# Kernel optimization log

Hardware: AMD Instinct MI355X
Metric: run time of the kernel (lower is better)

## Reference

```python
import jax, jax.numpy as jnp
import numpy as np

# module hyperparameters (from init_kwargs)
DELTA_T = 300
K = 16
FS = 30
HIGH_PASS = 40  # bpm
LOW_PASS = 250  # bpm

# static frequency band selection: rfft length F = DELTA_T//2 + 1
_F = DELTA_T // 2 + 1
_freqs = np.linspace(0.0, FS / 2.0, _F)
_sel = np.nonzero((_freqs >= HIGH_PASS / 60.0) & (_freqs <= LOW_PASS / 60.0))[0]
SEL_LO, SEL_HI = int(_sel[0]), int(_sel[-1]) + 1  # contiguous band -> static slice


def setup_inputs() -> dict:
    key = jax.random.key(0)
    k1, k2 = jax.random.split(key)
    B, C, T = 128, 32, 9000
    x = jax.random.normal(k1, (B, C, T), dtype=jnp.float32)
    offsets = jax.random.randint(k2, (B, C, K), 0, T - DELTA_T + 1, dtype=jnp.int32)
    return {"x": x, "offsets": offsets}


def reference(x, offsets):
    # x: [B, C, T], offsets: [B, C, K] in [0, T - DELTA_T]
    # Gather K random windows of length DELTA_T per (b, c).
    idx = offsets[..., None] + jnp.arange(DELTA_T, dtype=offsets.dtype)  # [B,C,K,DT]
    w = jnp.take_along_axis(x[:, :, None, :], idx, axis=-1)             # [B,C,K,DT]
    # mean-subtract along time
    w = w - jnp.mean(w, axis=-1, keepdims=True)
    # rfft with norm='forward' (divide by N), power spectrum
    spec = jnp.fft.rfft(w, axis=-1, norm="forward")                     # [B,C,K,F]
    p = spec.real ** 2 + spec.imag ** 2
    # static band selection (freqs in [HIGH_PASS/60, LOW_PASS/60] Hz)
    p = p[..., SEL_LO:SEL_HI]                                           # [B,C,K,35]
    # normalize to unit sum -> normalized PSD
    return p / jnp.sum(p, axis=-1, keepdims=True)
```

## Files before the change

kernel.cpp:

```cpp
#include <hip/hip_runtime.h>
#include <hip/hip_bf16.h>

using frag_ab = __attribute__((ext_vector_type(8))) short;
using f32x4   = __attribute__((ext_vector_type(4))) float;
typedef float f32x4u __attribute__((ext_vector_type(4), aligned(4)));


struct CS { double c[300]; double s[300]; };

constexpr CS make_cs() {
    CS t{};
    const double PI = 3.14159265358979323846;
    for (int m = 0; m < 300; ++m) {
        int q = m / 75, r = m % 75;
        double th = PI * (double)r / 150.0;
        double x2 = th * th;
        double term = 1.0, cv = 0.0;
        for (int k2 = 0; k2 < 12; ++k2) { cv += term; term *= -x2 / ((2*k2+1)*(2*k2+2)); }
        double sv = 0.0; term = th;
        for (int k2 = 0; k2 < 12; ++k2) { sv += term; term *= -x2 / ((2*k2+2)*(2*k2+3)); }
        double cc = 0.0, ss = 0.0;
        if      (q == 0) { cc =  cv; ss =  sv; }
        else if (q == 1) { cc = -sv; ss =  cv; }
        else if (q == 2) { cc = -cv; ss = -sv; }
        else             { cc =  sv; ss = -cv; }
        t.c[m] = cc; t.s[m] = ss;
    }
    return t;
}
constexpr CS TAB = make_cs();

constexpr unsigned short d2bf(double v) {
    unsigned s = 0; double a = v;
    if (a < 0) { s = 1; a = -a; }
    if (a < 1e-8) return 0;
    int e = 0;
    while (a >= 2.0) { a *= 0.5; ++e; }
    while (a <  1.0) { a *= 2.0; --e; }
    double m = (a - 1.0) * 128.0;
    int mi = (int)(m + 0.5);
    int ef = 127 + e;
    if (mi == 128) { mi = 0; ++ef; }
    return (unsigned short)((s << 15) | ((unsigned)ef << 7) | (unsigned)mi);
}

struct alignas(16) Chunk { unsigned short v[2560]; };

constexpr Chunk make_chunk(int kc) {
    Chunk ch{};
    for (int i = 0; i < 2560; ++i) {
        int e = i & 7, l = (i >> 3) & 63, n = i >> 9;
        int k   = kc * 32 + ((l >> 4) << 3) + e;
        int col = n * 16 + (l & 15);
        double v = 0.0;
        if (k < 300 && col < 70) {
            int j = (col < 35) ? col : col - 35;
            int m = ((7 + j) * k) % 300;
            v = (col < 35) ? TAB.c[m] : TAB.s[m];
        }
        ch.v[i] = d2bf(v);
    }
    return ch;
}

__device__ constexpr Chunk BP0 = make_chunk(0);
__device__ constexpr Chunk BP1 = make_chunk(1);
__device__ constexpr Chunk BP2 = make_chunk(2);
__device__ constexpr Chunk BP3 = make_chunk(3);
__device__ constexpr Chunk BP4 = make_chunk(4);
__device__ constexpr Chunk BP5 = make_chunk(5);
__device__ constexpr Chunk BP6 = make_chunk(6);
__device__ constexpr Chunk BP7 = make_chunk(7);
__device__ constexpr Chunk BP8 = make_chunk(8);
__device__ constexpr Chunk BP9 = make_chunk(9);

__device__ __forceinline__ const unsigned short* bp_ptr(int kc) {
    switch (kc) {
        case 0: return BP0.v; case 1: return BP1.v; case 2: return BP2.v;
        case 3: return BP3.v; case 4: return BP4.v; case 5: return BP5.v;
        case 6: return BP6.v; case 7: return BP7.v; case 8: return BP8.v;
        default: return BP9.v;
    }
}

__device__ __forceinline__ unsigned short f2bf(float f) {
    unsigned u = __float_as_uint(f);
    u += 0x7fffu + ((u >> 16) & 1u);
    return (unsigned short)(u >> 16);
}

__global__ __launch_bounds__(256) void st_spec_main(
    const float* __restrict__ x, const int* __restrict__ offs,
    float* __restrict__ out)
{
    const int tid  = threadIdx.x;
    const int wave = tid >> 6;
    const int lane = tid & 63;
    const int bc   = blockIdx.x * 4 + wave;
    const int c16  = lane & 15;
    const int kq   = lane >> 4;

    const float* xrow = x + (size_t)bc * 9000;
    const int off = offs[bc * 16 + c16];

    frag_ab a[10];
    #pragma unroll
    for (int kc = 0; kc < 9; ++kc) {
        const float* p = xrow + off + kc * 32 + kq * 8;
        f32x4u v0 = *(const f32x4u*)p;
        f32x4u v1 = *(const f32x4u*)(p + 4);
        frag_ab av;
        #pragma unroll
        for (int e = 0; e < 4; ++e) av[e] = (short)f2bf(v0[e]);
        #pragma unroll
        for (int e = 0; e < 4; ++e) av[4 + e] = (short)f2bf(v1[e]);
        a[kc] = av;
    }
    {
        int tb = 288 + kq * 8;
        frag_ab av;
        #pragma unroll
        for (int e = 0; e < 8; ++e) {
            int t = tb + e;
            av[e] = (short)f2bf((t < 300) ? xrow[off + t] : 0.0f);
        }
        a[9] = av;
    }

    f32x4 acc[5];
    #pragma unroll
    for (int n = 0; n < 5; ++n) acc[n] = (f32x4){0.f, 0.f, 0.f, 0.f};

    #pragma unroll
    for (int kc = 0; kc < 10; ++kc) {
        const unsigned short* bp = bp_ptr(kc);
        #pragma unroll
        for (int n = 0; n < 5; ++n) {
            frag_ab b = *(const frag_ab*)&bp[(n * 64 + lane) * 8];
            acc[n] = __builtin_amdgcn_mfma_f32_16x16x32_bf16(a[kc], b, acc[n], 0, 0, 0);
        }
    }

    const int src = (lane & 48) | ((c16 + 3) & 15);
    #pragma unroll
    for (int r = 0; r < 4; ++r) {
        float re0 = acc[0][r], re1 = acc[1][r], re2 = acc[2][r];
        float sh2 = __shfl(acc[2][r], src);
        float sh3 = __shfl(acc[3][r], src);
        float sh4 = __shfl(acc[4][r], src);
        float im0 = (c16 < 13) ? sh2 : sh3;
        float im1 = (c16 < 13) ? sh3 : sh4;
        float p0 = re0 * re0 + im0 * im0;
        float p1 = re1 * re1 + im1 * im1;
        float p2 = (c16 < 3) ? (re2 * re2 + sh4 * sh4) : 0.0f;
        float ps = p0 + p1 + p2;
        ps += __shfl_xor(ps, 1);
        ps += __shfl_xor(ps, 2);
        ps += __shfl_xor(ps, 4);
        ps += __shfl_xor(ps, 8);
        float inv = 1.0f / ps;
        int row = kq * 4 + r;
        float* orow = out + ((size_t)bc * 16 + row) * 35;
        orow[c16]      = p0 * inv;
        orow[16 + c16] = p1 * inv;
        if (c16 < 3) orow[32 + c16] = p2 * inv;
    }
}

extern "C" void kernel_launch(void* const* d_in, const int* in_sizes, int n_in,
                              void* d_out, int out_size, void* d_ws, size_t ws_size,
                              hipStream_t stream) {
    const float* x    = (const float*)d_in[0];
    const int*   offs = (const int*)d_in[1];
    float*       out  = (float*)d_out;
    hipLaunchKernelGGL(st_spec_main, dim3(1024), dim3(256), 0, stream,
                       x, offs, out);
}
```

Before: 23.79 us.

## Stage DFT basis in LDS, use packed bf16 convert, 512-thread blocks

```diff
diff --git a/kernel.cpp b/kernel.cpp
--- a/kernel.cpp
+++ b/kernel.cpp
@@ -3,7 +3,9 @@
 
 using frag_ab = __attribute__((ext_vector_type(8))) short;
 using f32x4   = __attribute__((ext_vector_type(4))) float;
+using i32x4   = __attribute__((ext_vector_type(4))) int;
 typedef float f32x4u __attribute__((ext_vector_type(4), aligned(4)));
+using u16x8   = __attribute__((ext_vector_type(8))) unsigned short;
 
 
 struct CS { double c[300]; double s[300]; };
@@ -63,40 +65,37 @@
     return ch;
 }
 
-__device__ constexpr Chunk BP0 = make_chunk(0);
-__device__ constexpr Chunk BP1 = make_chunk(1);
-__device__ constexpr Chunk BP2 = make_chunk(2);
-__device__ constexpr Chunk BP3 = make_chunk(3);
-__device__ constexpr Chunk BP4 = make_chunk(4);
-__device__ constexpr Chunk BP5 = make_chunk(5);
-__device__ constexpr Chunk BP6 = make_chunk(6);
-__device__ constexpr Chunk BP7 = make_chunk(7);
-__device__ constexpr Chunk BP8 = make_chunk(8);
-__device__ constexpr Chunk BP9 = make_chunk(9);
+__device__ constexpr Chunk BPALL[10] = {
+    make_chunk(0), make_chunk(1), make_chunk(2), make_chunk(3), make_chunk(4),
+    make_chunk(5), make_chunk(6), make_chunk(7), make_chunk(8), make_chunk(9)
+};
 
-__device__ __forceinline__ const unsigned short* bp_ptr(int kc) {
-    switch (kc) {
-        case 0: return BP0.v; case 1: return BP1.v; case 2: return BP2.v;
-        case 3: return BP3.v; case 4: return BP4.v; case 5: return BP5.v;
-        case 6: return BP6.v; case 7: return BP7.v; case 8: return BP8.v;
-        default: return BP9.v;
-    }
+__device__ __forceinline__ unsigned cvtpk(float lo, float hi) {
+    unsigned r;
+    asm("v_cvt_pk_bf16_f32 %0, %1, %2" : "=v"(r) : "v"(lo), "v"(hi));
+    return r;
 }
 
-__device__ __forceinline__ unsigned short f2bf(float f) {
-    unsigned u = __float_as_uint(f);
-    u += 0x7fffu + ((u >> 16) & 1u);
-    return (unsigned short)(u >> 16);
-}
-
-__global__ __launch_bounds__(256) void st_spec_main(
+__global__ __launch_bounds__(512) void st_spec_main(
     const float* __restrict__ x, const int* __restrict__ offs,
     float* __restrict__ out)
 {
-    const int tid  = threadIdx.x;
+    __shared__ __align__(16) unsigned short Bp[25600];
+
+    const int tid = threadIdx.x;
+
+    {
+        const u16x8* src = (const u16x8*)&BPALL[0];
+        u16x8* dst = (u16x8*)Bp;
+        #pragma unroll
+        for (int i = 0; i < 6; ++i) dst[tid + i * 512] = src[tid + i * 512];
+        int i6 = tid + 6 * 512;
+        if (i6 < 3200) dst[i6] = src[i6];
+    }
+
     const int wave = tid >> 6;
     const int lane = tid & 63;
-    const int bc   = blockIdx.x * 4 + wave;
+    const int bc   = blockIdx.x * 8 + wave;
     const int c16  = lane & 15;
     const int kq   = lane >> 4;
 
@@ -109,23 +108,30 @@
         const float* p = xrow + off + kc * 32 + kq * 8;
         f32x4u v0 = *(const f32x4u*)p;
         f32x4u v1 = *(const f32x4u*)(p + 4);
-        frag_ab av;
-        #pragma unroll
-        for (int e = 0; e < 4; ++e) av[e] = (short)f2bf(v0[e]);
-        #pragma unroll
-        for (int e = 0; e < 4; ++e) av[4 + e] = (short)f2bf(v1[e]);
-        a[kc] = av;
+        i32x4 w;
+        w[0] = cvtpk(v0[0], v0[1]);
+        w[1] = cvtpk(v0[2], v0[3]);
+        w[2] = cvtpk(v1[0], v1[1]);
+        w[3] = cvtpk(v1[2], v1[3]);
+        a[kc] = __builtin_bit_cast(frag_ab, w);
     }
     {
         int tb = 288 + kq * 8;
-        frag_ab av;
+        float v[8];
         #pragma unroll
         for (int e = 0; e < 8; ++e) {
             int t = tb + e;
-            av[e] = (short)f2bf((t < 300) ? xrow[off + t] : 0.0f);
+            v[e] = (t < 300) ? xrow[off + t] : 0.0f;
         }
-        a[9] = av;
+        i32x4 w;
+        w[0] = cvtpk(v[0], v[1]);
+        w[1] = cvtpk(v[2], v[3]);
+        w[2] = cvtpk(v[4], v[5]);
+        w[3] = cvtpk(v[6], v[7]);
+        a[9] = __builtin_bit_cast(frag_ab, w);
     }
+
+    __syncthreads();
 
     f32x4 acc[5];
     #pragma unroll
@@ -133,10 +139,9 @@
 
     #pragma unroll
     for (int kc = 0; kc < 10; ++kc) {
-        const unsigned short* bp = bp_ptr(kc);
         #pragma unroll
         for (int n = 0; n < 5; ++n) {
-            frag_ab b = *(const frag_ab*)&bp[(n * 64 + lane) * 8];
+            frag_ab b = *(const frag_ab*)&Bp[((kc * 5 + n) * 64 + lane) * 8];
             acc[n] = __builtin_amdgcn_mfma_f32_16x16x32_bf16(a[kc], b, acc[n], 0, 0, 0);
         }
     }
@@ -173,6 +178,6 @@
     const float* x    = (const float*)d_in[0];
     const int*   offs = (const int*)d_in[1];
     float*       out  = (float*)d_out;
-    hipLaunchKernelGGL(st_spec_main, dim3(1024), dim3(256), 0, stream,
+    hipLaunchKernelGGL(st_spec_main, dim3(512), dim3(512), 0, stream,
                        x, offs, out);
 }
```

Result: faster. 20.42 us (-14.1%).
